# Performance work log

Hardware: AMD Instinct MI355X
Metric: run time of the kernel (lower is better)

Reference implementation:

```python
import jax, jax.numpy as jnp
import numpy as np
from jax import lax

N_ITERS = 50
FETCH_K_RATIO = 9.0 / 8.0
EPS = 1.0


def coor_descent(s, n_iters, k, eps):
    # s: [B, N] routing scores; k: scalar effective-k (float)
    logk = jnp.log(jnp.asarray(k, s.dtype))
    a0 = jnp.zeros(s.shape[:-1] + (1,), s.dtype)
    b0 = -s

    def step(carry, _):
        a, b = carry
        sb = (s + b) / eps
        a = eps * (logk - jax.nn.logsumexp(sb, axis=-1, keepdims=True))
        b = -jax.nn.relu(s + a)
        return (a, b), None

    (a, b), _ = lax.scan(step, (a0, b0), None, length=n_iters)
    return jnp.exp((s + a + b) / eps)


def setup_inputs() -> dict:
    key = jax.random.key(0)
    k1, k2 = jax.random.split(key)
    B, N, D = 8, 8192, 2048
    x = jax.random.normal(k1, (B, N, D), dtype=jnp.float32)
    routing_token = jax.random.normal(k2, (1, D), dtype=jnp.float32)
    return {"x": x, "routing_token": routing_token, "num_tokens": 1024}


def reference(x, routing_token, num_tokens):
    # x: [B, N, D], routing_token: [R=1, D]
    n = x.shape[-2]
    # s: [B, R, N] -> pack to [B*R, N] (R=1)
    s = jnp.einsum("bnd,rd->brn", x, routing_token)
    s = s.reshape(-1, n)
    effective_k = min(num_tokens * FETCH_K_RATIO, n)
    scores = coor_descent(s, N_ITERS, effective_k, EPS)  # [B, N]
    selected_scores, selected_indices = lax.top_k(scores, num_tokens)
    # straight-through: value -> 1, gradient flows through selected_scores
    selected_scores = selected_scores + lax.stop_gradient(1.0 - selected_scores)
    return selected_scores, selected_indices
```

## Files before the change

kernel.cpp:

```cpp
#include <hip/hip_runtime.h>
#include <stdint.h>
#include <math.h>

#define BB 8
#define NN 8192
#define DD 2048
#define NITERS 50
#define NTHR 512
#define EPT 16

typedef float f32x4 __attribute__((ext_vector_type(4)));

__global__ __launch_bounds__(256) void gemv_k(const float* __restrict__ x,
                                              const float* __restrict__ r,
                                              float* __restrict__ s) {
    const int wid  = threadIdx.x >> 6;
    const int lane = threadIdx.x & 63;
    const int wv   = blockIdx.x * 4 + wid;

    f32x4 w[8];
#pragma unroll
    for (int j = 0; j < 8; ++j) w[j] = *reinterpret_cast<const f32x4*>(r + (j * 64 + lane) * 4);

#pragma unroll
    for (int g = 0; g < 4; ++g) {
        const int row = wv * 2 + g * 16384;
        const float* x0 = x + (size_t)row * DD;
        float a0 = 0.f, a1 = 0.f;
#pragma unroll
        for (int j = 0; j < 8; ++j) {
            const int idx = (j * 64 + lane) * 4;
            const f32x4 v0 = *reinterpret_cast<const f32x4*>(x0 + idx);
            const f32x4 v1 = *reinterpret_cast<const f32x4*>(x0 + DD + idx);
            a0 = fmaf(v0.x, w[j].x, a0); a0 = fmaf(v0.y, w[j].y, a0);
            a0 = fmaf(v0.z, w[j].z, a0); a0 = fmaf(v0.w, w[j].w, a0);
            a1 = fmaf(v1.x, w[j].x, a1); a1 = fmaf(v1.y, w[j].y, a1);
            a1 = fmaf(v1.z, w[j].z, a1); a1 = fmaf(v1.w, w[j].w, a1);
        }
#pragma unroll
        for (int off = 32; off > 0; off >>= 1) {
            a0 += __shfl_xor(a0, off, 64);
            a1 += __shfl_xor(a1, off, 64);
        }
        if (lane == 0) { s[row] = a0; s[row + 1] = a1; }
    }
}

__global__ __launch_bounds__(NTHR) void router_k(const float* __restrict__ s_in,
                                                 const int* __restrict__ ntok_p,
                                                 float* __restrict__ out) {
    __shared__ uint64_t keys[NN];
    __shared__ __align__(16) float fscr[2][8];
    __shared__ int iscr[8];

    const int row  = blockIdx.x;
    const int tid  = threadIdx.x;
    const int lane = tid & 63;
    const int wid  = tid >> 6;
    const int ntok = ntok_p[0];

    const float LOG2E = 1.4426950408889634f;
    const float* sp = s_in + (size_t)row * NN;
    float p[EPT];
#pragma unroll
    for (int c = 0; c < 4; ++c) {
        const f32x4 v = *reinterpret_cast<const f32x4*>(sp + tid * EPT + c * 4);
        p[c * 4 + 0] = __builtin_exp2f(v.x * LOG2E);
        p[c * 4 + 1] = __builtin_exp2f(v.y * LOG2E);
        p[c * 4 + 2] = __builtin_exp2f(v.z * LOG2E);
        p[c * 4 + 3] = __builtin_exp2f(v.w * LOG2E);
    }

    const float logk2 = __builtin_log2f(fminf((float)ntok * 1.125f, (float)NN));
    float a2 = logk2 - 13.0f;

    for (int it = 1; it < NITERS; ++it) {
        const float A = __builtin_exp2f(a2);
        float e[EPT];
#pragma unroll
        for (int j = 0; j < EPT; ++j) e[j] = fminf(p[j] * A, 1.0f);
#pragma unroll
        for (int st = 1; st < EPT; st <<= 1)
#pragma unroll
            for (int j = 0; j < EPT; j += 2 * st) e[j] += e[j + st];
        float u = e[0];
#pragma unroll
        for (int off = 32; off > 0; off >>= 1) u += __shfl_xor(u, off, 64);
        float* buf = fscr[it & 1];
        if (lane == 0) buf[wid] = u;
        __syncthreads();
        const f32x4 p0 = *reinterpret_cast<const f32x4*>(&buf[0]);
        const f32x4 p1 = *reinterpret_cast<const f32x4*>(&buf[4]);
        const float U = ((p0.x + p0.y) + (p0.z + p0.w)) + ((p1.x + p1.y) + (p1.z + p1.w));
        a2 = (logk2 - __builtin_log2f(U)) + a2;
    }

    const float A = __builtin_exp2f(a2);
    int flags = 0, cnt_m = 0;
#pragma unroll
    for (int j = 0; j < EPT; ++j) {
        if (fminf(p[j] * A, 1.0f) == 1.0f) { flags |= (1 << j); ++cnt_m; }
    }

    int xsc = cnt_m;
#pragma unroll
    for (int off = 1; off < 64; off <<= 1) {
        const int y = __shfl_up(xsc, off, 64);
        if (lane >= off) xsc += y;
    }
    if (lane == 63) iscr[wid] = xsc;
    __syncthreads();
    int wbase = 0, total = 0;
#pragma unroll
    for (int w2 = 0; w2 < 8; ++w2) {
        const int t = iscr[w2];
        if (w2 < wid) wbase += t;
        total += t;
    }
    const int base = wbase + (xsc - cnt_m);

    float* out1 = out + (size_t)BB * ntok;

    for (int q = tid; q < ntok; q += NTHR) out[(size_t)row * ntok + q] = 1.0f;

    if (total >= ntok) {
        int pos = base;
#pragma unroll
        for (int j = 0; j < EPT; ++j) {
            if (flags & (1 << j)) {
                if (pos < ntok) out1[(size_t)row * ntok + pos] = (float)(tid * EPT + j);
                ++pos;
            }
        }
    } else {
        __syncthreads();
#pragma unroll
        for (int j = 0; j < EPT; ++j) {
            const float e2 = fminf(p[j] * A, 1.0f);
            const uint32_t bits = __float_as_uint(e2);
            keys[tid * EPT + j] =
                ((uint64_t)bits << 32) | (uint32_t)(0xFFFFFFFFu - (uint32_t)(tid * EPT + j));
        }
        __syncthreads();
        for (unsigned k = 2; k <= NN; k <<= 1) {
            for (unsigned jj = k >> 1; jj > 0; jj >>= 1) {
                for (unsigned q = tid; q < NN / 2; q += NTHR) {
                    const unsigned i   = ((q & ~(jj - 1)) << 1) | (q & (jj - 1));
                    const unsigned ixj = i | jj;
                    const bool up = ((i & k) == 0);
                    const uint64_t ka = keys[i], kb = keys[ixj];
                    if ((ka < kb) == up) { keys[i] = kb; keys[ixj] = ka; }
                }
                __syncthreads();
            }
        }
        for (int q = tid; q < ntok; q += NTHR) {
            const uint32_t idx = 0xFFFFFFFFu - (uint32_t)(keys[q] & 0xFFFFFFFFull);
            out1[(size_t)row * ntok + q] = (float)idx;
        }
    }
}

extern "C" void kernel_launch(void* const* d_in, const int* in_sizes, int n_in,
                              void* d_out, int out_size, void* d_ws, size_t ws_size,
                              hipStream_t stream) {
    const float* x = (const float*)d_in[0];
    const float* r = (const float*)d_in[1];
    const int* ntok = (const int*)d_in[2];
    float* out = (float*)d_out;
    float* s = (float*)d_ws;

    gemv_k<<<2048, 256, 0, stream>>>(x, r, s);
    router_k<<<BB, NTHR, 0, stream>>>(s, ntok, out);
}
```

Baseline: 127.1 us.

## Double-buffer GEMV rows through LDS with async global_load_lds staging

The GEMV kernel now streams x rows into per-wave LDS double buffers using 16-byte global_load_lds. The next row is prefetched while the current one is reduced, with explicit vmcnt waits to order the buffers. Each wave now handles one row per batch across eight batches, instead of two adjacent rows across four groups. The goal is to keep more memory traffic in flight and overlap loads with compute. In exchange each block uses 64 KB of LDS, which limits occupancy, and correctness depends on hand-counted vmcnt values.

```diff
diff --git a/kernel.cpp b/kernel.cpp
--- a/kernel.cpp
+++ b/kernel.cpp
@@ -10,10 +10,17 @@
 #define EPT 16
 
 typedef float f32x4 __attribute__((ext_vector_type(4)));
+typedef __attribute__((address_space(3))) uint32_t lds_u32_t;
+typedef __attribute__((address_space(1))) const uint32_t glb_u32_t;
+
+__device__ __forceinline__ void stage16(const float* g, float* l) {
+    __builtin_amdgcn_global_load_lds((glb_u32_t*)g, (lds_u32_t*)l, 16, 0, 0);
+}
 
 __global__ __launch_bounds__(256) void gemv_k(const float* __restrict__ x,
                                               const float* __restrict__ r,
                                               float* __restrict__ s) {
+    __shared__ float xs[4][2][DD];
     const int wid  = threadIdx.x >> 6;
     const int lane = threadIdx.x & 63;
     const int wv   = blockIdx.x * 4 + wid;
@@ -22,27 +29,43 @@
 #pragma unroll
     for (int j = 0; j < 8; ++j) w[j] = *reinterpret_cast<const f32x4*>(r + (j * 64 + lane) * 4);
 
+    const float* xw = x + (size_t)wv * DD;
+    float* lb0 = &xs[wid][0][0];
+    float* lb1 = &xs[wid][1][0];
+
 #pragma unroll
-    for (int g = 0; g < 4; ++g) {
-        const int row = wv * 2 + g * 16384;
-        const float* x0 = x + (size_t)row * DD;
-        float a0 = 0.f, a1 = 0.f;
+    for (int c = 0; c < 8; ++c) stage16(xw + c * 256 + lane * 4, lb0 + c * 256);
+
+#pragma unroll
+    for (int g = 0; g < 8; ++g) {
+        float* cur = (g & 1) ? lb1 : lb0;
+        float* nxt = (g & 1) ? lb0 : lb1;
+        if (g < 7) {
+            const float* xn = xw + (size_t)(g + 1) * NN * DD;
+#pragma unroll
+            for (int c = 0; c < 8; ++c) stage16(xn + c * 256 + lane * 4, nxt + c * 256);
+        }
+        if (g == 0)      asm volatile("s_waitcnt vmcnt(8)" ::: "memory");
+        else if (g == 7) asm volatile("s_waitcnt vmcnt(1)" ::: "memory");
+        else             asm volatile("s_waitcnt vmcnt(9)" ::: "memory");
+        __builtin_amdgcn_sched_barrier(0);
+
+        float accA = 0.f, accB = 0.f;
 #pragma unroll
         for (int j = 0; j < 8; ++j) {
-            const int idx = (j * 64 + lane) * 4;
-            const f32x4 v0 = *reinterpret_cast<const f32x4*>(x0 + idx);
-            const f32x4 v1 = *reinterpret_cast<const f32x4*>(x0 + DD + idx);
-            a0 = fmaf(v0.x, w[j].x, a0); a0 = fmaf(v0.y, w[j].y, a0);
-            a0 = fmaf(v0.z, w[j].z, a0); a0 = fmaf(v0.w, w[j].w, a0);
-            a1 = fmaf(v1.x, w[j].x, a1); a1 = fmaf(v1.y, w[j].y, a1);
-            a1 = fmaf(v1.z, w[j].z, a1); a1 = fmaf(v1.w, w[j].w, a1);
+            const f32x4 v = *reinterpret_cast<const f32x4*>(cur + (j * 64 + lane) * 4);
+            if (j < 4) {
+                accA = fmaf(v.x, w[j].x, accA); accA = fmaf(v.y, w[j].y, accA);
+                accA = fmaf(v.z, w[j].z, accA); accA = fmaf(v.w, w[j].w, accA);
+            } else {
+                accB = fmaf(v.x, w[j].x, accB); accB = fmaf(v.y, w[j].y, accB);
+                accB = fmaf(v.z, w[j].z, accB); accB = fmaf(v.w, w[j].w, accB);
+            }
         }
+        float acc = accA + accB;
 #pragma unroll
-        for (int off = 32; off > 0; off >>= 1) {
-            a0 += __shfl_xor(a0, off, 64);
-            a1 += __shfl_xor(a1, off, 64);
-        }
-        if (lane == 0) { s[row] = a0; s[row + 1] = a1; }
+        for (int off = 32; off > 0; off >>= 1) acc += __shfl_xor(acc, off, 64);
+        if (lane == 0) s[wv + g * NN] = acc;
     }
 }
 
```

Measured after the change: 124.4 us. -2.2%, faster.
